# Kernel tuning notes

Measured on AMD Instinct MI355X. Metric: run time of the kernel, lower is better.

The kernel has to match this reference:

```python
import jax, jax.numpy as jnp
import numpy as np

DIM = 1024
HEADS = 16
HEAD_DIM = DIM // HEADS
EPS = 1e-5


def setup_inputs() -> dict:
    key = jax.random.key(0)
    ks = jax.random.split(key, 4)
    N, L = 4, 2048
    x = jax.random.normal(ks[0], (N, L, DIM), dtype=jnp.float32)
    # causal mask: True means masked (strictly upper triangle)
    attn_mask = jnp.triu(jnp.ones((L, L), dtype=jnp.bool_), k=1)[None, None, :, :]
    w_qkv = jax.random.normal(ks[1], (3 * DIM, DIM), dtype=jnp.float32) * (DIM ** -0.5)
    w_proj = jax.random.normal(ks[2], (DIM, DIM), dtype=jnp.float32) * (DIM ** -0.5)
    b_proj = jnp.zeros((DIM,), dtype=jnp.float32)
    q_gamma = jnp.ones((HEAD_DIM,), dtype=jnp.float32)
    q_beta = jnp.zeros((HEAD_DIM,), dtype=jnp.float32)
    k_gamma = jnp.ones((HEAD_DIM,), dtype=jnp.float32)
    k_beta = jnp.zeros((HEAD_DIM,), dtype=jnp.float32)
    return {"x": x, "attn_mask": attn_mask, "w_qkv": w_qkv, "w_proj": w_proj,
            "b_proj": b_proj, "q_gamma": q_gamma, "q_beta": q_beta,
            "k_gamma": k_gamma, "k_beta": k_beta}


def _layernorm(h, gamma, beta):
    mu = jnp.mean(h, axis=-1, keepdims=True)
    var = jnp.mean(jnp.square(h - mu), axis=-1, keepdims=True)
    return (h - mu) * jax.lax.rsqrt(var + EPS) * gamma + beta


def reference(x, attn_mask, w_qkv, w_proj, b_proj, q_gamma, q_beta, k_gamma, k_beta):
    N, L, D = x.shape
    H, hd = HEADS, HEAD_DIM
    scale = hd ** -0.5
    qkv = jnp.einsum('nld,ed->nle', x, w_qkv)  # [N, L, 3D]
    qkv = qkv.reshape(N, L, 3, H, hd).transpose(2, 0, 3, 1, 4)  # [3, N, H, L, hd]
    q, k, v = qkv[0], qkv[1], qkv[2]
    q = _layernorm(q, q_gamma, q_beta)
    k = _layernorm(k, k_gamma, k_beta)
    scores = jnp.einsum('nhqd,nhkd->nhqk', q * scale, k)
    scores = scores + jnp.where(attn_mask, -jnp.inf, 0.0).astype(scores.dtype)
    attn = jax.nn.softmax(scores, axis=-1)
    out = jnp.einsum('nhqk,nhkd->nhqd', attn, v)  # [N, H, L, hd]
    out = out.transpose(0, 2, 1, 3).reshape(N, L, D)
    return jnp.einsum('nld,ed->nle', out, w_proj) + b_proj
```

## Files before the change

kernel.cpp:

```cpp
#include <hip/hip_runtime.h>


using f16x8 = __attribute__((ext_vector_type(8))) _Float16;
using f16x4 = __attribute__((ext_vector_type(4))) _Float16;
using f16x2 = __attribute__((ext_vector_type(2))) _Float16;
using f32x4 = __attribute__((ext_vector_type(4))) float;
using f32x16 = __attribute__((ext_vector_type(16))) float;
using u32x4 = __attribute__((ext_vector_type(4))) unsigned int;

#define MFMA16(a, b, c) __builtin_amdgcn_mfma_f32_16x16x32_f16(a, b, c, 0, 0, 0)
#define MFMA32(a, b, c) __builtin_amdgcn_mfma_f32_32x32x16_f16(a, b, c, 0, 0, 0)

__device__ __forceinline__ void gload_lds16(const void* g, void* l) {
  __builtin_amdgcn_global_load_lds(
      (const __attribute__((address_space(1))) unsigned int*)g,
      (__attribute__((address_space(3))) unsigned int*)l, 16, 0, 0);
}

__device__ __forceinline__ float dot2acc(unsigned int pk, float c) {
#if __has_builtin(__builtin_amdgcn_fdot2)
  const f16x2 ones = {(_Float16)1.f, (_Float16)1.f};
  return __builtin_amdgcn_fdot2(__builtin_bit_cast(f16x2, pk), ones, c, false);
#else
  f16x2 v = __builtin_bit_cast(f16x2, pk);
  return c + (float)v[0] + (float)v[1];
#endif
}

__global__ __launch_bounds__(256) void convert_all_kernel(
    const float* __restrict__ x, const float* __restrict__ wq,
    const float* __restrict__ wp, _Float16* __restrict__ xb,
    _Float16* __restrict__ wqb, _Float16* __restrict__ wpb) {
  long i = ((long)blockIdx.x * 256 + threadIdx.x) * 8;
  const float* src;
  _Float16* dst;
  if (i < 8388608) {
    src = x; dst = xb;
  } else if (i < 8388608 + 3145728) {
    src = wq + (i - 8388608); dst = wqb + (i - 8388608); i = 0;
  } else {
    src = wp + (i - 11534336); dst = wpb + (i - 11534336); i = 0;
  }
  float4 a = *(const float4*)(src + i);
  float4 b = *(const float4*)(src + i + 4);
  f16x8 o;
  o[0] = (_Float16)a.x; o[1] = (_Float16)a.y; o[2] = (_Float16)a.z; o[3] = (_Float16)a.w;
  o[4] = (_Float16)b.x; o[5] = (_Float16)b.y; o[6] = (_Float16)b.z; o[7] = (_Float16)b.w;
  *(f16x8*)(dst + i) = o;
}

template <int MODE>
__global__ __launch_bounds__(256, 2) void gemm_bt(
    const _Float16* __restrict__ A, const _Float16* __restrict__ B,
    void* __restrict__ Cout, _Float16* __restrict__ Vt,
    const float* __restrict__ bias,
    const float* __restrict__ qg, const float* __restrict__ qb,
    const float* __restrict__ kg, const float* __restrict__ kb,
    int M, int N, int K) {
  __shared__ __align__(16) char smem[73728];
  const int tid = threadIdx.x;
  const int w = tid >> 6, lane = tid & 63;
  const int c = lane & 15, g = lane >> 4;
  const long mbase = (long)blockIdx.x * 128;
  const int nby = (MODE == 1) ? 12 : 4;
  const int by = (MODE == 1) ? (int)((blockIdx.y + 8) % 12) : (int)blockIdx.y;
  const long nbase = (long)by * 256;
  const int wm = (w >> 1) * 64, wn = (w & 1) * 128;
  const int sr4 = lane >> 2;
  const int scol = ((lane & 3) ^ ((lane >> 3) & 3)) * 8;
  const int sg = (g ^ ((c >> 1) & 3)) * 8;
  const char* pAr = smem + (wm + c) * 64 + sg * 2;
  const char* pBr = smem + 24576 + (wn + c) * 64 + sg * 2;
  (void)nby;

#define GSTAGE(aOff_, bOff_, kt_)                                             \
  {                                                                           \
    const int kk_ = (kt_) * 32;                                               \
    _Pragma("unroll") for (int i = 0; i < 2; ++i) {                           \
      const int arow = w * 32 + i * 16 + sr4;                                 \
      gload_lds16(A + (mbase + arow) * K + kk_ + scol,                        \
                  smem + (aOff_) + (w * 2 + i) * 1024);                       \
    }                                                                         \
    _Pragma("unroll") for (int j = 0; j < 4; ++j) {                           \
      const int brow = w * 64 + j * 16 + sr4;                                 \
      gload_lds16(B + (nbase + brow) * K + kk_ + scol,                        \
                  smem + 24576 + (bOff_) + (w * 4 + j) * 1024);               \
    }                                                                         \
  }

  f32x4 acc[4][8];
#pragma unroll
  for (int i = 0; i < 4; ++i)
#pragma unroll
    for (int j = 0; j < 8; ++j) acc[i][j] = f32x4{0.f, 0.f, 0.f, 0.f};

  const int nk = K >> 5;
  GSTAGE(0, 0, 0);
  GSTAGE(8192, 16384, 1);
  int aR = 0, bR = 0;
  int aS = 16384, bS = 32768;
  for (int kt = 0; kt < nk; ++kt) {
    if (kt + 1 < nk) {
      asm volatile("s_waitcnt vmcnt(6)" ::: "memory");
    } else {
      asm volatile("s_waitcnt vmcnt(0)" ::: "memory");
    }
    __builtin_amdgcn_sched_barrier(0);
    __builtin_amdgcn_s_barrier();
    __builtin_amdgcn_sched_barrier(0);
    f16x8 af[4], bfr[8];
#pragma unroll
    for (int mt = 0; mt < 4; ++mt)
      af[mt] = *(const f16x8*)(pAr + aR + mt * 1024);
#pragma unroll
    for (int nt = 0; nt < 8; ++nt)
      bfr[nt] = *(const f16x8*)(pBr + bR + nt * 1024);
    if (kt + 2 < nk) GSTAGE(aS, bS, kt + 2);
#pragma unroll
    for (int mt = 0; mt < 4; ++mt)
#pragma unroll
      for (int nt = 0; nt < 8; ++nt)
        acc[mt][nt] = MFMA16(af[mt], bfr[nt], acc[mt][nt]);
    aR = (aR == 16384) ? 0 : aR + 8192;
    bR = (bR == 32768) ? 0 : bR + 16384;
    aS = (aS == 16384) ? 0 : aS + 8192;
    bS = (bS == 32768) ? 0 : bS + 16384;
  }
#undef GSTAGE

  if constexpr (MODE == 1) {
    const int region = by >> 2;
    if (region == 2) {
      __syncthreads();
      _Float16* T = (_Float16*)smem;
#pragma unroll
      for (int nt = 0; nt < 8; ++nt) {
        const int dloc = wn + nt * 16 + c;
#pragma unroll
        for (int mt = 0; mt < 4; ++mt) {
          const int lloc = wm + mt * 16 + g * 4;
          f16x4 o;
#pragma unroll
          for (int r = 0; r < 4; ++r) o[r] = (_Float16)acc[mt][nt][r];
          *(f16x4*)(T + dloc * 136 + lloc) = o;
        }
      }
      __syncthreads();
      const long n = mbase >> 11;
      const long lbase = mbase & 2047;
      const int chunk = tid & 15;
      const int rbase = tid >> 4;
#pragma unroll
      for (int i = 0; i < 16; ++i) {
        const int row = rbase + i * 16;
        const long dcol = (nbase - 2048) + row;
        *(f16x8*)(Vt + (n * 1024 + dcol) * 2048 + lbase + chunk * 8) =
            *(const f16x8*)(T + row * 136 + chunk * 8);
      }
      return;
    }
    const float* gamma = region ? kg : qg;
    const float* beta = region ? kb : qb;
    float gam[4], bet[4];
#pragma unroll
    for (int j = 0; j < 4; ++j) {
      gam[j] = gamma[j * 16 + c];
      bet[j] = beta[j * 16 + c];
    }
    const float sc = region ? 1.f : 0.1803368801111204f;
#pragma unroll
    for (int mt = 0; mt < 4; ++mt)
#pragma unroll
      for (int hh = 0; hh < 2; ++hh)
#pragma unroll
        for (int r = 0; r < 4; ++r) {
          float s1 = 0.f, s2 = 0.f;
#pragma unroll
          for (int j = 0; j < 4; ++j) {
            const float v = acc[mt][hh * 4 + j][r];
            s1 += v;
            s2 += v * v;
          }
#pragma unroll
          for (int msk = 1; msk < 16; msk <<= 1) {
            s1 += __shfl_xor(s1, msk);
            s2 += __shfl_xor(s2, msk);
          }
          const float mu = s1 * 0.015625f;
          const float rstd = rsqrtf(s2 * 0.015625f - mu * mu + 1e-5f);
#pragma unroll
          for (int j = 0; j < 4; ++j)
            acc[mt][hh * 4 + j][r] =
                ((acc[mt][hh * 4 + j][r] - mu) * rstd * gam[j] + bet[j]) * sc;
        }
#pragma unroll
    for (int nt = 0; nt < 8; ++nt) {
      const long col = nbase + wn + nt * 16 + c;
#pragma unroll
      for (int mt = 0; mt < 4; ++mt)
#pragma unroll
        for (int r = 0; r < 4; ++r) {
          const long row = mbase + wm + mt * 16 + g * 4 + r;
          ((_Float16*)Cout)[row * N + col] = (_Float16)acc[mt][nt][r];
        }
    }
  } else {
#pragma unroll
    for (int nt = 0; nt < 8; ++nt) {
      const long col = nbase + wn + nt * 16 + c;
      const float bv = bias ? bias[col] : 0.f;
#pragma unroll
      for (int mt = 0; mt < 4; ++mt)
#pragma unroll
        for (int r = 0; r < 4; ++r) {
          const long row = mbase + wm + mt * 16 + g * 4 + r;
          ((float*)Cout)[row * N + col] = acc[mt][nt][r] + bv;
        }
    }
  }
}

__global__ __launch_bounds__(256, 4) void attn_kernel(
    const _Float16* __restrict__ qkv, const _Float16* __restrict__ Vt,
    _Float16* __restrict__ Ob) {
  __shared__ __align__(16) char lds[32768];
  const int w = threadIdx.x >> 6;
  const int lane = threadIdx.x & 63;
  const int c5 = lane & 31;
  const int hi = lane >> 5;
  const int nh = blockIdx.x;
  const long n = nh >> 4;
  const int h = nh & 15;
  const int qtile = 15 - blockIdx.y;
  const int qlo_blk = qtile * 128;
  const int qlo = qlo_blk + w * 32;
  const int qrow = qlo + c5;

  const _Float16* Qp = qkv + n * 2048 * 3072 + h * 64;
  const _Float16* Kq = Qp + 1024;
  const _Float16* Vp = Vt + (long)nh * 64 * 2048;

  const int sr8 = lane >> 3;
  const int scol = ((lane & 7) ^ sr8) * 8;

  const int nkv_blk = (qlo_blk + 191) >> 6;
  const int nkv_w = (qlo + 95) >> 6;

#define STAGE(BUF, kv_)                                                        \
  {                                                                            \
    const int kb_ = (kv_) * 64;                                                \
    _Pragma("unroll") for (int i = 0; i < 2; ++i) {                            \
      const int idx = w * 2 + i;                                               \
      const int row = idx * 8 + sr8;                                           \
      gload_lds16(Kq + (long)(kb_ + row) * 3072 + scol,                        \
                  lds + (BUF) * 8192 + idx * 1024);                            \
      gload_lds16(Vp + (long)row * 2048 + kb_ + scol,                          \
                  lds + 16384 + (BUF) * 8192 + idx * 1024);                    \
    }                                                                          \
  }

  f16x8 qf[4];
#pragma unroll
  for (int dc = 0; dc < 4; ++dc)
    qf[dc] = *(const f16x8*)(Qp + (long)qrow * 3072 + dc * 16 + hi * 8);

  f32x16 negM;
#pragma unroll
  for (int r = 0; r < 16; ++r) negM[r] = -12.0f;

  f32x16 acc[2];
#pragma unroll
  for (int db = 0; db < 2; ++db)
#pragma unroll
    for (int r = 0; r < 16; ++r) acc[db][r] = 0.f;
  float ls = 0.f;

  const int swr = c5 & 7;
  const char* Lb[4];
#pragma unroll
  for (int j = 0; j < 4; ++j)
    Lb[j] = lds + c5 * 128 + (((j * 2 + hi) ^ swr) << 4);

#define COMPUTE(BUF, kv_)                                                      \
  {                                                                            \
    const int kbase = (kv_) * 64;                                              \
    f32x16 s0, s1;                                                             \
    __builtin_amdgcn_s_setprio(1);                                             \
    {                                                                          \
      f16x8 kf0 = *(const f16x8*)(Lb[0] + (BUF) * 8192);                       \
      f16x8 kf1 = *(const f16x8*)(Lb[0] + (BUF) * 8192 + 4096);                \
      s0 = MFMA32(kf0, qf[0], negM);                                           \
      s1 = MFMA32(kf1, qf[0], negM);                                           \
    }                                                                          \
    _Pragma("unroll") for (int dc = 1; dc < 4; ++dc) {                         \
      f16x8 kf0 = *(const f16x8*)(Lb[dc] + (BUF) * 8192);                      \
      f16x8 kf1 = *(const f16x8*)(Lb[dc] + (BUF) * 8192 + 4096);               \
      s0 = MFMA32(kf0, qf[dc], s0);                                            \
      s1 = MFMA32(kf1, qf[dc], s1);                                            \
    }                                                                          \
    __builtin_amdgcn_s_setprio(0);                                             \
    if (kbase + 63 > qlo) {                                                    \
      _Pragma("unroll") for (int r = 0; r < 16; ++r) {                         \
        const int mv = (r & 3) + 8 * (r >> 2) + 4 * hi;                        \
        if (kbase + mv > qrow) s0[r] = -1e30f;                                 \
        if (kbase + 32 + mv > qrow) s1[r] = -1e30f;                            \
      }                                                                        \
    }                                                                          \
    _Pragma("unroll") for (int r = 0; r < 16; ++r) {                           \
      s0[r] = exp2f(s0[r]);                                                    \
      s1[r] = exp2f(s1[r]);                                                    \
    }                                                                          \
    unsigned int pk0[4][2], pk1[4][2];                                         \
    _Pragma("unroll") for (int r2 = 0; r2 < 4; ++r2)                           \
        _Pragma("unroll") for (int p = 0; p < 2; ++p) {                        \
      pk0[r2][p] = __builtin_bit_cast(                                         \
          unsigned int, __builtin_amdgcn_cvt_pkrtz(s0[4 * r2 + 2 * p],         \
                                                   s0[4 * r2 + 2 * p + 1]));   \
      pk1[r2][p] = __builtin_bit_cast(                                         \
          unsigned int, __builtin_amdgcn_cvt_pkrtz(s1[4 * r2 + 2 * p],         \
                                                   s1[4 * r2 + 2 * p + 1]));   \
    }                                                                          \
    _Pragma("unroll") for (int r2 = 0; r2 < 4; ++r2)                           \
        _Pragma("unroll") for (int p = 0; p < 2; ++p) {                        \
      ls = dot2acc(pk0[r2][p], ls);                                            \
      ls = dot2acc(pk1[r2][p], ls);                                            \
    }                                                                          \
    f16x8 pB[4];                                                               \
    _Pragma("unroll") for (int kk = 0; kk < 4; ++kk) {                         \
      const int rx = (kk & 1) * 2;                                             \
      unsigned int x0 = (kk < 2) ? pk0[rx][0] : pk1[rx][0];                    \
      unsigned int y0 = (kk < 2) ? pk0[rx + 1][0] : pk1[rx + 1][0];            \
      unsigned int x1 = (kk < 2) ? pk0[rx][1] : pk1[rx][1];                    \
      unsigned int y1 = (kk < 2) ? pk0[rx + 1][1] : pk1[rx + 1][1];            \
      asm("v_permlane32_swap_b32 %0, %1" : "+v"(x0), "+v"(y0));                \
      asm("v_permlane32_swap_b32 %0, %1" : "+v"(x1), "+v"(y1));                \
      pB[kk] = __builtin_bit_cast(f16x8, u32x4{x0, x1, y0, y1});               \
    }                                                                          \
    __builtin_amdgcn_s_setprio(1);                                             \
    _Pragma("unroll") for (int db = 0; db < 2; ++db)                           \
        _Pragma("unroll") for (int kk = 0; kk < 4; ++kk) {                     \
      f16x8 vf = *(const f16x8*)(Lb[kk] + 16384 + (BUF) * 8192 + db * 4096);   \
      acc[db] = MFMA32(vf, pB[kk], acc[db]);                                   \
    }                                                                          \
    __builtin_amdgcn_s_setprio(0);                                             \
  }

  STAGE(0, 0);
  for (int kv = 0; kv < nkv_blk; kv += 2) {
    __syncthreads();
    if (kv + 1 < nkv_blk) STAGE(1, kv + 1);
    if (kv < nkv_w) COMPUTE(0, kv);
    if (kv + 1 >= nkv_blk) break;
    __syncthreads();
    if (kv + 2 < nkv_blk) STAGE(0, kv + 2);
    if (kv + 1 < nkv_w) COMPUTE(1, kv + 1);
  }
#undef COMPUTE
#undef STAGE

  const float lsr = ls + __shfl_xor(ls, 32);
  const float inv = 1.f / lsr;
  _Float16* ob = Ob + ((long)(n * 2048) + qrow) * 1024 + h * 64 + 4 * hi;
#pragma unroll
  for (int db = 0; db < 2; ++db)
#pragma unroll
    for (int r2 = 0; r2 < 4; ++r2) {
      f16x4 o;
#pragma unroll
      for (int j = 0; j < 4; ++j)
        o[j] = (_Float16)(acc[db][4 * r2 + j] * inv);
      *(f16x4*)(ob + db * 32 + 8 * r2) = o;
    }
}

extern "C" void kernel_launch(void* const* d_in, const int* in_sizes, int n_in,
                              void* d_out, int out_size, void* d_ws, size_t ws_size,
                              hipStream_t stream) {
  const float* x = (const float*)d_in[0];
  const float* w_qkv = (const float*)d_in[2];
  const float* w_proj = (const float*)d_in[3];
  const float* b_proj = (const float*)d_in[4];
  const float* qg = (const float*)d_in[5];
  const float* qb = (const float*)d_in[6];
  const float* kg = (const float*)d_in[7];
  const float* kb = (const float*)d_in[8];

  char* ws = (char*)d_ws;
  _Float16* xb     = (_Float16*)(ws + 0);
  _Float16* wqkvb  = (_Float16*)(ws + 16777216);
  _Float16* wprojb = (_Float16*)(ws + 23068672);
  _Float16* qkvh   = (_Float16*)(ws + 25165824);
  _Float16* Vt     = (_Float16*)(ws + 75497472);
  _Float16* Ob     = xb;

  convert_all_kernel<<<6144, 256, 0, stream>>>(x, w_qkv, w_proj,
                                               xb, wqkvb, wprojb);

  gemm_bt<1><<<dim3(64, 12), 256, 0, stream>>>(xb, wqkvb, qkvh, Vt, nullptr,
                                               qg, qb, kg, kb, 8192, 3072, 1024);
  attn_kernel<<<dim3(64, 16), 256, 0, stream>>>(qkvh, Vt, Ob);
  gemm_bt<0><<<dim3(64, 4), 256, 0, stream>>>(Ob, wprojb, d_out, nullptr, b_proj,
                                              nullptr, nullptr, nullptr, nullptr,
                                              8192, 1024, 1024);
}
```

Baseline: 189.7 us.

## Shrink GEMM LDS to double buffering and split V transpose epilogue in halves

Cuts the GEMM's shared-memory pipeline from three stages to two (73.7KB to 48KB), so prefetch of tile kt+1 is issued after a full vmcnt(0) wait each iteration. The V-transpose epilogue is split into two passes over half the columns so the staging buffer fits the smaller LDS. The aim is to let more blocks fit per CU (launch bounds ask for 2) at the cost of a shallower load/compute overlap and extra barriers in the epilogue.

```diff
diff --git a/kernel.cpp b/kernel.cpp
--- a/kernel.cpp
+++ b/kernel.cpp
@@ -57,12 +57,11 @@
     const float* __restrict__ qg, const float* __restrict__ qb,
     const float* __restrict__ kg, const float* __restrict__ kb,
     int M, int N, int K) {
-  __shared__ __align__(16) char smem[73728];
+  __shared__ __align__(16) char smem[49152];
   const int tid = threadIdx.x;
   const int w = tid >> 6, lane = tid & 63;
   const int c = lane & 15, g = lane >> 4;
   const long mbase = (long)blockIdx.x * 128;
-  const int nby = (MODE == 1) ? 12 : 4;
   const int by = (MODE == 1) ? (int)((blockIdx.y + 8) % 12) : (int)blockIdx.y;
   const long nbase = (long)by * 256;
   const int wm = (w >> 1) * 64, wn = (w & 1) * 128;
@@ -70,21 +69,20 @@
   const int scol = ((lane & 3) ^ ((lane >> 3) & 3)) * 8;
   const int sg = (g ^ ((c >> 1) & 3)) * 8;
   const char* pAr = smem + (wm + c) * 64 + sg * 2;
-  const char* pBr = smem + 24576 + (wn + c) * 64 + sg * 2;
-  (void)nby;
-
-#define GSTAGE(aOff_, bOff_, kt_)                                             \
+  const char* pBr = smem + 16384 + (wn + c) * 64 + sg * 2;
+
+#define GSTAGE(buf, kt_)                                                      \
   {                                                                           \
     const int kk_ = (kt_) * 32;                                               \
     _Pragma("unroll") for (int i = 0; i < 2; ++i) {                           \
       const int arow = w * 32 + i * 16 + sr4;                                 \
       gload_lds16(A + (mbase + arow) * K + kk_ + scol,                        \
-                  smem + (aOff_) + (w * 2 + i) * 1024);                       \
+                  smem + (buf) * 8192 + (w * 2 + i) * 1024);                  \
     }                                                                         \
     _Pragma("unroll") for (int j = 0; j < 4; ++j) {                           \
       const int brow = w * 64 + j * 16 + sr4;                                 \
       gload_lds16(B + (nbase + brow) * K + kk_ + scol,                        \
-                  smem + 24576 + (bOff_) + (w * 4 + j) * 1024);               \
+                  smem + 16384 + (buf) * 16384 + (w * 4 + j) * 1024);         \
     }                                                                         \
   }
 
@@ -95,36 +93,26 @@
     for (int j = 0; j < 8; ++j) acc[i][j] = f32x4{0.f, 0.f, 0.f, 0.f};
 
   const int nk = K >> 5;
-  GSTAGE(0, 0, 0);
-  GSTAGE(8192, 16384, 1);
-  int aR = 0, bR = 0;
-  int aS = 16384, bS = 32768;
+  GSTAGE(0, 0);
   for (int kt = 0; kt < nk; ++kt) {
-    if (kt + 1 < nk) {
-      asm volatile("s_waitcnt vmcnt(6)" ::: "memory");
-    } else {
-      asm volatile("s_waitcnt vmcnt(0)" ::: "memory");
-    }
+    const int cur = kt & 1;
+    asm volatile("s_waitcnt vmcnt(0)" ::: "memory");
     __builtin_amdgcn_sched_barrier(0);
     __builtin_amdgcn_s_barrier();
     __builtin_amdgcn_sched_barrier(0);
+    if (kt + 1 < nk) GSTAGE(cur ^ 1, kt + 1);
     f16x8 af[4], bfr[8];
 #pragma unroll
     for (int mt = 0; mt < 4; ++mt)
-      af[mt] = *(const f16x8*)(pAr + aR + mt * 1024);
+      af[mt] = *(const f16x8*)(pAr + cur * 8192 + mt * 1024);
 #pragma unroll
     for (int nt = 0; nt < 8; ++nt)
-      bfr[nt] = *(const f16x8*)(pBr + bR + nt * 1024);
-    if (kt + 2 < nk) GSTAGE(aS, bS, kt + 2);
+      bfr[nt] = *(const f16x8*)(pBr + cur * 16384 + nt * 1024);
 #pragma unroll
     for (int mt = 0; mt < 4; ++mt)
 #pragma unroll
       for (int nt = 0; nt < 8; ++nt)
         acc[mt][nt] = MFMA16(af[mt], bfr[nt], acc[mt][nt]);
-    aR = (aR == 16384) ? 0 : aR + 8192;
-    bR = (bR == 32768) ? 0 : bR + 16384;
-    aS = (aS == 16384) ? 0 : aS + 8192;
-    bS = (bS == 32768) ? 0 : bS + 16384;
   }
 #undef GSTAGE
 
@@ -133,29 +121,35 @@
     if (region == 2) {
       __syncthreads();
       _Float16* T = (_Float16*)smem;
-#pragma unroll
-      for (int nt = 0; nt < 8; ++nt) {
-        const int dloc = wn + nt * 16 + c;
-#pragma unroll
-        for (int mt = 0; mt < 4; ++mt) {
-          const int lloc = wm + mt * 16 + g * 4;
-          f16x4 o;
-#pragma unroll
-          for (int r = 0; r < 4; ++r) o[r] = (_Float16)acc[mt][nt][r];
-          *(f16x4*)(T + dloc * 136 + lloc) = o;
-        }
-      }
-      __syncthreads();
       const long n = mbase >> 11;
       const long lbase = mbase & 2047;
       const int chunk = tid & 15;
       const int rbase = tid >> 4;
 #pragma unroll
-      for (int i = 0; i < 16; ++i) {
-        const int row = rbase + i * 16;
-        const long dcol = (nbase - 2048) + row;
-        *(f16x8*)(Vt + (n * 1024 + dcol) * 2048 + lbase + chunk * 8) =
-            *(const f16x8*)(T + row * 136 + chunk * 8);
+      for (int p = 0; p < 2; ++p) {
+        if ((w & 1) == p) {
+#pragma unroll
+          for (int nt = 0; nt < 8; ++nt) {
+            const int dloc = nt * 16 + c;
+#pragma unroll
+            for (int mt = 0; mt < 4; ++mt) {
+              const int lloc = wm + mt * 16 + g * 4;
+              f16x4 o;
+#pragma unroll
+              for (int r = 0; r < 4; ++r) o[r] = (_Float16)acc[mt][nt][r];
+              *(f16x4*)(T + dloc * 136 + lloc) = o;
+            }
+          }
+        }
+        __syncthreads();
+#pragma unroll
+        for (int i = 0; i < 8; ++i) {
+          const int row = rbase + i * 16;
+          const long dcol = (nbase - 2048) + p * 128 + row;
+          *(f16x8*)(Vt + (n * 1024 + dcol) * 2048 + lbase + chunk * 8) =
+              *(const f16x8*)(T + row * 136 + chunk * 8);
+        }
+        __syncthreads();
       }
       return;
     }
```

New measurement: 194.2 us. +2.4%, slower.
